# Optimization experiments

Measured on AMD Instinct MI355X. Metric: run time of the kernel, lower is better.

## Reference

```python
import jax, jax.numpy as jnp
import numpy as np
import math
from itertools import combinations

SEQ_LEN = 8
D_MODEL = 2048
OUT_DIM = 1152
WAY = 5
SHOT = 5
N_SUPPORT = WAY * SHOT
N_QUERIES = 200
TUPLES = np.array(list(combinations(range(SEQ_LEN), 2)), dtype=np.int32)  # [28, 2]
L = TUPLES.shape[0]  # 28 temporal tuples
PE_SCALE = 0.1
LN_EPS = 1e-5
COS_EPS = 1e-8


def _pos_encoding(seq, d):
    pos = jnp.arange(seq, dtype=jnp.float32)[:, None]
    div = jnp.exp(jnp.arange(0, d, 2, dtype=jnp.float32) * (-math.log(10000.0) / d))
    pe = jnp.zeros((seq, d), dtype=jnp.float32)
    pe = pe.at[:, 0::2].set(jnp.sin(pos * div) * PE_SCALE)
    pe = pe.at[:, 1::2].set(jnp.cos(pos * div) * PE_SCALE)
    return pe  # [seq, d]


def _layernorm(x, g, b):
    mu = x.mean(-1, keepdims=True)
    var = ((x - mu) ** 2).mean(-1, keepdims=True)
    return (x - mu) * jax.lax.rsqrt(var + LN_EPS) * g + b


def setup_inputs() -> dict:
    key = jax.random.key(0)
    ks = jax.random.split(key, 6)
    support_set = jax.random.normal(ks[0], (N_SUPPORT, SEQ_LEN, D_MODEL), jnp.float32)
    queries = jax.random.normal(ks[1], (N_QUERIES, SEQ_LEN, D_MODEL), jnp.float32)
    # sorted equal-shot episode: labels = [0]*5 + [1]*5 + ... + [4]*5
    support_labels = jnp.repeat(jnp.arange(WAY, dtype=jnp.int32), SHOT)
    k_w = jax.random.normal(ks[2], (OUT_DIM, 2 * D_MODEL), jnp.float32) * 0.02
    v_w = jax.random.normal(ks[3], (OUT_DIM, 2 * D_MODEL), jnp.float32) * 0.02
    k_b = jnp.zeros((OUT_DIM,), jnp.float32)
    v_b = jnp.zeros((OUT_DIM,), jnp.float32)
    ln_k_g = jnp.ones((OUT_DIM,), jnp.float32)
    ln_k_b = jnp.zeros((OUT_DIM,), jnp.float32)
    return {"support_set": support_set, "support_labels": support_labels,
            "queries": queries, "k_w": k_w, "k_b": k_b, "v_w": v_w, "v_b": v_b,
            "ln_k_g": ln_k_g, "ln_k_b": ln_k_b}


def reference(support_set, support_labels, queries, k_w, k_b, v_w, v_b, ln_k_g, ln_k_b):
    # dropout is inference-mode (identity)
    pe = _pos_encoding(SEQ_LEN, D_MODEL)
    sp = support_set + pe  # [Ns, S, D_MODEL]
    qp = queries + pe      # [Nq, S, D_MODEL]

    tup = jnp.asarray(TUPLES)
    # gather temporal tuples: [N, L, 2, D_MODEL] -> [N, L, 2*D_MODEL]
    s_t = sp[:, tup].reshape(N_SUPPORT, L, 2 * D_MODEL)
    q_t = qp[:, tup].reshape(N_QUERIES, L, 2 * D_MODEL)

    ks_s = _layernorm(s_t @ k_w.T + k_b, ln_k_g, ln_k_b)  # [Ns, L, OUT]
    ks_q = _layernorm(q_t @ k_w.T + k_b, ln_k_g, ln_k_b)  # [Nq, L, OUT]
    vs_s = s_t @ v_w.T + v_b                               # [Ns, L, OUT] (no norm, per original)
    vs_q = q_t @ v_w.T + v_b                               # [Nq, L, OUT]

    # labels are sorted equal-shot -> group by class via reshape
    ks_c = ks_s.reshape(WAY, SHOT, L, OUT_DIM)
    vs_c = vs_s.reshape(WAY, SHOT, L, OUT_DIM)

    # attention scores: [WAY, Nq, L(query tuple), SHOT, L(support tuple)]
    scores = jnp.einsum('qld,wsed->wqlse', ks_q, ks_c) / math.sqrt(OUT_DIM)
    attn = jax.nn.softmax(scores.reshape(WAY, N_QUERIES, L, SHOT * L), axis=-1)
    attn = attn.reshape(WAY, N_QUERIES, L, SHOT, L)
    # prototype: sum over shot of attn @ class_v -> [WAY, Nq, L, OUT]
    proto = jnp.einsum('wqlse,wsed->wqld', attn, vs_c)

    # query logits: -||q_v - proto||_F^2 / L per class
    diff = vs_q[None] - proto  # [WAY, Nq, L, OUT]
    ori = (-(diff ** 2).sum(axis=(-2, -1)) / L).T  # [Nq, WAY]

    # all_distances_tensor [Nq, L*OUT, WAY]
    A = jnp.transpose(proto, (1, 2, 3, 0)).reshape(N_QUERIES, L * OUT_DIM, WAY)
    num = jnp.einsum('qda,qdb->qab', A, A)            # [Nq, WAY, WAY]
    nrm = jnp.sqrt((A * A).sum(axis=1))               # [Nq, WAY]
    den = jnp.maximum(nrm[:, :, None] * nrm[:, None, :], COS_EPS)
    sim = num / den                                    # [Nq, WAY, WAY]
    return sim, ori
```

## Files before the change

kernel.cpp:

```cpp
#include <hip/hip_runtime.h>
#include <hip/hip_bf16.h>
#include <math.h>

typedef __hip_bfloat16 bf16;
typedef short s16x8 __attribute__((ext_vector_type(8)));
typedef float f32x4 __attribute__((ext_vector_type(4)));

#define NQ 200
#define SEQ 8
#define DM 2048
#define OUTD 1152
#define LT 28
#define M_ALL 6300
#define SM 5600
#define SN_PAD 768
#define ATT_STRIDE 720
#define N2 2304
#define KP 160
#define CH_Q 50
#define CH_ROWS 1400
#define CH_MPAD 1408
#define ABLK 144

__device__ __forceinline__ float bf2f(bf16 v) { return __bfloat162float(v); }
__device__ __forceinline__ bf16 f2bf(float v) { return __float2bfloat16(v); }
__device__ __forceinline__ float ubits2f(unsigned int u16) {
    unsigned int i = u16 << 16;
    float f; __builtin_memcpy(&f, &i, 4); return f;
}
__device__ __forceinline__ unsigned short f2bits(float f) {
    bf16 b = __float2bfloat16(f);
    unsigned short u; __builtin_memcpy(&u, &b, 2); return u;
}

__device__ const int TUP_A[LT] = {0,0,0,0,0,0,0,1,1,1,1,1,1,2,2,2,2,2,3,3,3,3,4,4,4,5,5,6};
__device__ const int TUP_B[LT] = {1,2,3,4,5,6,7,2,3,4,5,6,7,3,4,5,6,7,4,5,6,7,5,6,7,6,7,7};

__global__ __launch_bounds__(256) void wconv2_k(const float4* __restrict__ kw,
                                                const float4* __restrict__ vw,
                                                ushort4* __restrict__ o) {
    int i = blockIdx.x * 256 + threadIdx.x;
    float4 v = (i < 1179648) ? kw[i] : vw[i - 1179648];
    ushort4 r;
    r.x = f2bits(v.x); r.y = f2bits(v.y); r.z = f2bits(v.z); r.w = f2bits(v.w);
    o[i] = r;
}

__global__ __launch_bounds__(256) void pe_k(float* __restrict__ pe,
                                            bf16* __restrict__ attn_tail) {
    int i = blockIdx.x * 256 + threadIdx.x;
    int s = i >> 11, d = i & 2047;
    float dv = expf((float)(d & ~1) * (-9.210340371976184f / 2048.0f));
    float ang = (float)s * dv;
    pe[i] = (d & 1) ? cosf(ang) * 0.1f : sinf(ang) * 0.1f;
    for (int j = i; j < 32 * ATT_STRIDE; j += 64 * 256) attn_tail[j] = f2bf(0.f);
}

__global__ __launch_bounds__(256) void pex_k(const float* __restrict__ sup,
                                             const float* __restrict__ qry,
                                             const float* __restrict__ pe,
                                             bf16* __restrict__ pexb) {
    int r = blockIdx.x, t = threadIdx.x;
    int n, s;
    const float* src;
    if (r < 200) { n = r >> 3; s = r & 7; src = sup; }
    else { int rr = r - 200; n = rr >> 3; s = rr & 7; src = qry; }
    const float4* row = (const float4*)(src + ((size_t)n * SEQ + s) * DM);
    const float4* per = (const float4*)(pe + (size_t)s * DM);
    ushort4* orow = (ushort4*)(pexb + (size_t)r * DM);
    for (int d = t; d < DM / 4; d += 256) {
        float4 a = row[d], p = per[d];
        ushort4 o;
        o.x = f2bits(a.x + p.x); o.y = f2bits(a.y + p.y);
        o.z = f2bits(a.z + p.z); o.w = f2bits(a.w + p.w);
        orow[d] = o;
    }
}

__global__ __launch_bounds__(256) void gemm_bt(
    const bf16* __restrict__ A, int lda, size_t aZ,
    const bf16* __restrict__ B, int ldb, size_t bZ,
    float scale, bf16* __restrict__ C, int ldc, size_t cZ, int K, int mlim) {
    const int gx = gridDim.x, gy = gridDim.y;
    const int nwg = gx * gy * (int)gridDim.z;
    const int orig = ((int)blockIdx.z * gy + blockIdx.y) * gx + blockIdx.x;
    const int qc = nwg >> 3, rc = nwg & 7;
    const int xcd = orig & 7, sub = orig >> 3;
    const int lg = (xcd < rc ? xcd * (qc + 1) : rc * (qc + 1) + (xcd - rc) * qc) + sub;
    const int bx = lg % gx;
    const int rest = lg / gx;
    const int by = rest % gy, bz = rest / gy;

    const unsigned short* Ag0 = (const unsigned short*)A + aZ * bz;
    const unsigned short* Bg0 = (const unsigned short*)B + bZ * bz;
    const size_t cbase = cZ * bz;
    const int tile_m = bx * 128, tile_n = by * 128;
    __shared__ unsigned short A0s[4096];
    __shared__ unsigned short A1s[4096];
    __shared__ unsigned short B0s[4096];
    __shared__ unsigned short B1s[4096];
    const int t = threadIdx.x, lane = t & 63, wave = t >> 6;
    const int wm = (wave & 1) * 64, wn = (wave >> 1) * 64;
    const int srow = t >> 1, sq0 = (t & 1) * 2;
    const unsigned short* Ag = Ag0 + (size_t)(tile_m + srow) * lda + (t & 1) * 16;
    const unsigned short* Bg = Bg0 + (size_t)(tile_n + srow) * ldb + (t & 1) * 16;
    const int offW0 = ((sq0 + 0) * 128 + srow) * 8;
    const int offW1 = ((sq0 + 1) * 128 + srow) * 8;
    const int fr = lane & 15, quad = lane >> 4;

    f32x4 acc[4][4];
#pragma unroll
    for (int i = 0; i < 4; i++)
#pragma unroll
        for (int j = 0; j < 4; j++) acc[i][j] = {0.f, 0.f, 0.f, 0.f};

    uint4 ra0, ra1, rb0, rb1;
#define GLOAD(k0) do {                                                          \
    ra0 = *(const uint4*)(Ag + (k0));  ra1 = *(const uint4*)(Ag + (k0) + 8);    \
    rb0 = *(const uint4*)(Bg + (k0));  rb1 = *(const uint4*)(Bg + (k0) + 8);    \
  } while (0)

#define LDSW(AS, BS) do {                                                       \
    *(uint4*)&AS[offW0] = ra0; *(uint4*)&AS[offW1] = ra1;                       \
    *(uint4*)&BS[offW0] = rb0; *(uint4*)&BS[offW1] = rb1;                       \
  } while (0)

#define COMPUTE(AS, BS) do {                                                    \
    s16x8 af[4], bfv[4];                                                        \
    _Pragma("unroll")                                                           \
    for (int i = 0; i < 4; i++)                                                 \
        af[i] = *(const s16x8*)&AS[(quad * 128 + wm + i * 16 + fr) * 8];        \
    _Pragma("unroll")                                                           \
    for (int j = 0; j < 4; j++)                                                 \
        bfv[j] = *(const s16x8*)&BS[(quad * 128 + wn + j * 16 + fr) * 8];       \
    _Pragma("unroll")                                                           \
    for (int i = 0; i < 4; i++)                                                 \
    _Pragma("unroll")                                                           \
        for (int j = 0; j < 4; j++)                                             \
            acc[i][j] = __builtin_amdgcn_mfma_f32_16x16x32_bf16(af[i], bfv[j], acc[i][j], 0, 0, 0); \
  } while (0)

    const int nIter = K >> 5;
    GLOAD(0);
    LDSW(A0s, B0s);
    if (nIter > 1) GLOAD(32);
    __syncthreads();
    for (int s = 0; s < nIter; s += 2) {
        if (s + 1 < nIter) LDSW(A1s, B1s);
        if (s + 2 < nIter) GLOAD((s + 2) * 32);
        COMPUTE(A0s, B0s);
        __syncthreads();
        if (s + 1 < nIter) {
            if (s + 2 < nIter) LDSW(A0s, B0s);
            if (s + 3 < nIter) GLOAD((s + 3) * 32);
            COMPUTE(A1s, B1s);
            __syncthreads();
        }
    }
#undef GLOAD
#undef LDSW
#undef COMPUTE

    const int rb = quad * 4;
#pragma unroll
    for (int i = 0; i < 4; i++)
#pragma unroll
        for (int j = 0; j < 4; j++) {
            const int col = tile_n + wn + j * 16 + fr;
#pragma unroll
            for (int r = 0; r < 4; r++) {
                const int row = tile_m + wm + i * 16 + rb + r;
                if (row < mlim)
                    C[cbase + (size_t)row * ldc + col] = f2bf(acc[i][j][r] * scale);
            }
        }
}

__global__ __launch_bounds__(256) void combine_k(
    const unsigned int* __restrict__ Yk, const float* __restrict__ kb,
    const float* __restrict__ lng, const float* __restrict__ lnb,
    bf16* __restrict__ ks) {
    const int m = blockIdx.x, t = threadIdx.x, lane = t & 63, wave = t >> 6;
    int mm = m < 700 ? m : m - 700;
    int base = m < 700 ? 0 : 200;
    int nsamp = mm / LT, l = mm - nsamp * LT;
    const unsigned int* ya = Yk + (size_t)(base + nsamp * 8 + TUP_A[l]) * (N2 / 2);
    const unsigned int* yb = Yk + (size_t)(base + nsamp * 8 + TUP_B[l]) * (N2 / 2);
    float vals[5];
    int cnt = 0;
    float s = 0.f, s2 = 0.f;
    for (int n = t; n < OUTD; n += 256) {
        unsigned int ua = ya[n], ub = yb[n];
        float vk = ubits2f(ua & 0xFFFFu) + ubits2f(ub >> 16) + kb[n];
        vals[cnt++] = vk;
        s += vk; s2 += vk * vk;
    }
    for (int o = 32; o > 0; o >>= 1) { s += __shfl_xor(s, o); s2 += __shfl_xor(s2, o); }
    __shared__ float r1[4], r2[4];
    if (lane == 0) { r1[wave] = s; r2[wave] = s2; }
    __syncthreads();
    s = r1[0] + r1[1] + r1[2] + r1[3];
    s2 = r2[0] + r2[1] + r2[2] + r2[3];
    float mu = s * (1.f / OUTD);
    float var = s2 * (1.f / OUTD) - mu * mu;
    float inv = rsqrtf(fmaxf(var, 0.f) + 1e-5f);
    cnt = 0;
    for (int n = t; n < OUTD; n += 256)
        ks[(size_t)m * OUTD + n] = f2bf((vals[cnt++] - mu) * inv * lng[n] + lnb[n]);
}

__global__ __launch_bounds__(256) void combine_v(
    const unsigned int* __restrict__ Yv, const float* __restrict__ vb,
    bf16* __restrict__ vs) {
    const int m = blockIdx.x, t = threadIdx.x;
    int mm = m < 700 ? m : m - 700;
    int base = m < 700 ? 0 : 200;
    int nsamp = mm / LT, l = mm - nsamp * LT;
    const unsigned int* ya = Yv + (size_t)(base + nsamp * 8 + TUP_A[l]) * (N2 / 2);
    const unsigned int* yb = Yv + (size_t)(base + nsamp * 8 + TUP_B[l]) * (N2 / 2);
    for (int n = t; n < OUTD; n += 256) {
        unsigned int ua = ya[n], ub = yb[n];
        vs[(size_t)m * OUTD + n] =
            f2bf(ubits2f(ua & 0xFFFFu) + ubits2f(ub >> 16) + vb[n]);
    }
}

__global__ __launch_bounds__(320) void softmax_k(const bf16* __restrict__ sc,
                                                 bf16* __restrict__ attn) {
    const int row = blockIdx.x, w = threadIdx.x >> 6, lane = threadIdx.x & 63;
    const bf16* src = sc + (size_t)row * SN_PAD + w * 140;
    bf16* dst = attn + (size_t)row * ATT_STRIDE + w * ABLK;
    float a = bf2f(src[lane]);
    float b = bf2f(src[lane + 64]);
    float c = (lane < 12) ? bf2f(src[lane + 128]) : -3.0e38f;
    float m = fmaxf(fmaxf(a, b), c);
    for (int o = 32; o > 0; o >>= 1) m = fmaxf(m, __shfl_xor(m, o));
    float ea = __expf(a - m), eb = __expf(b - m);
    float ec = (lane < 12) ? __expf(c - m) : 0.f;
    float s = ea + eb + ec;
    for (int o = 32; o > 0; o >>= 1) s += __shfl_xor(s, o);
    float inv = 1.f / s;
    dst[lane] = f2bf(ea * inv);
    dst[lane + 64] = f2bf(eb * inv);
    if (lane < 16) dst[lane + 128] = f2bf(lane < 12 ? ec * inv : 0.f);
}

__global__ __launch_bounds__(256) void vspad_k(const bf16* __restrict__ vs,
                                               bf16* __restrict__ vp,
                                               float* __restrict__ gbuf) {
    int idx = blockIdx.x * 256 + threadIdx.x;
    if (blockIdx.x == 0)
        for (int i = threadIdx.x; i < NQ * 21; i += 256) gbuf[i] = 0.f;
    if (idx >= 5 * OUTD * KP) return;
    int j = idx % KP;
    int rest = idx / KP;
    int dcol = rest % OUTD;
    int w = rest / OUTD;
    vp[idx] = (j < 140) ? vs[(size_t)(w * 140 + j) * OUTD + dcol] : f2bf(0.f);
}

__global__ __launch_bounds__(256) void gramred_k(const bf16* __restrict__ protoc,
                                                 const bf16* __restrict__ vs,
                                                 float* __restrict__ gbuf,
                                                 int row0, int q0) {
    const int ql = blockIdx.x;
    const int lgb = blockIdx.y;
    const int t = threadIdx.x, lane = t & 63, wave = t >> 6;
    const size_t PZ = (size_t)CH_MPAD * OUTD;
    float g[15] = {0.f};
    float h[5] = {0.f, 0.f, 0.f, 0.f, 0.f};
    float e = 0.f;
    for (int idx = t; idx < 2 * OUTD / 8; idx += 256) {
        int li = idx / 144;
        int dv = idx - li * 144;
        int l = lgb * 2 + li;
        size_t ml = (size_t)(ql * LT + l) * OUTD + dv * 8;
        s16x8 pw0 = *(const s16x8*)&protoc[0 * PZ + ml];
        s16x8 pw1 = *(const s16x8*)&protoc[1 * PZ + ml];
        s16x8 pw2 = *(const s16x8*)&protoc[2 * PZ + ml];
        s16x8 pw3 = *(const s16x8*)&protoc[3 * PZ + ml];
        s16x8 pw4 = *(const s16x8*)&protoc[4 * PZ + ml];
        s16x8 vv = *(const s16x8*)&vs[(size_t)(700 + row0 + ql * LT + l) * OUTD + dv * 8];
#pragma unroll
        for (int ee = 0; ee < 8; ee++) {
            float pv[5];
            pv[0] = ubits2f((unsigned short)pw0[ee]);
            pv[1] = ubits2f((unsigned short)pw1[ee]);
            pv[2] = ubits2f((unsigned short)pw2[ee]);
            pv[3] = ubits2f((unsigned short)pw3[ee]);
            pv[4] = ubits2f((unsigned short)pw4[ee]);
            float v = ubits2f((unsigned short)vv[ee]);
            e += v * v;
            int c = 0;
#pragma unroll
            for (int a = 0; a < 5; a++) {
                h[a] += v * pv[a];
#pragma unroll
                for (int b = a; b < 5; b++) g[c++] += pv[a] * pv[b];
            }
        }
    }
    float vals[21];
#pragma unroll
    for (int k = 0; k < 15; k++) vals[k] = g[k];
#pragma unroll
    for (int k = 0; k < 5; k++) vals[15 + k] = h[k];
    vals[20] = e;
#pragma unroll
    for (int k = 0; k < 21; k++)
        for (int o = 32; o > 0; o >>= 1) vals[k] += __shfl_xor(vals[k], o);
    __shared__ float red[4][21];
    if (lane == 0)
#pragma unroll
        for (int k = 0; k < 21; k++) red[wave][k] = vals[k];
    __syncthreads();
    if (t < 21) {
        float s = red[0][t] + red[1][t] + red[2][t] + red[3][t];
        atomicAdd(&gbuf[(q0 + ql) * 21 + t], s);
    }
}

__global__ __launch_bounds__(64) void out_k(const float* __restrict__ gbuf,
                                            float* __restrict__ out) {
    int q = blockIdx.x;
    if (threadIdx.x != 0) return;
    const float* r = gbuf + q * 21;
    float G[5][5];
    int c = 0;
    for (int a = 0; a < 5; a++)
        for (int b = a; b < 5; b++) { G[a][b] = r[c]; G[b][a] = r[c]; c++; }
    float e = r[20];
    float nrm[5];
    for (int a = 0; a < 5; a++) nrm[a] = sqrtf(fmaxf(G[a][a], 0.f));
    for (int a = 0; a < 5; a++)
        for (int b = 0; b < 5; b++)
            out[(size_t)q * 25 + a * 5 + b] = G[a][b] / fmaxf(nrm[a] * nrm[b], 1e-8f);
    for (int w = 0; w < 5; w++)
        out[5000 + (size_t)q * 5 + w] = -(e - 2.f * r[15 + w] + G[w][w]) * (1.f / 28.f);
}

extern "C" void kernel_launch(void* const* d_in, const int* in_sizes, int n_in,
                              void* d_out, int out_size, void* d_ws, size_t ws_size,
                              hipStream_t stream) {
    const float* sup = (const float*)d_in[0];
    const float* qry = (const float*)d_in[2];
    const float* k_w = (const float*)d_in[3];
    const float* k_b = (const float*)d_in[4];
    const float* v_w = (const float*)d_in[5];
    const float* v_b = (const float*)d_in[6];
    const float* lng = (const float*)d_in[7];
    const float* lnb = (const float*)d_in[8];
    (void)in_sizes; (void)n_in; (void)out_size; (void)ws_size;

    char* ws = (char*)d_ws;
    bf16* pexb   = (bf16*)(ws + 0);
    bf16* wbf    = (bf16*)(ws + 7864320);
    bf16* Yk     = (bf16*)(ws + 26738688);
    bf16* Yv     = (bf16*)(ws + 35033088);
    bf16* ks     = (bf16*)(ws + 0);
    bf16* vs     = (bf16*)(ws + 16220160);
    bf16* sc     = (bf16*)(ws + 30735360);
    bf16* vsp    = (bf16*)(ws + 39386112);
    bf16* attn   = (bf16*)(ws + 41229312);
    float* gbuf  = (float*)(ws + 49339392);
    float* pe    = (float*)(ws + 49356192);
    bf16* protoc = (bf16*)(ws + 0);

    pe_k<<<dim3(64), dim3(256), 0, stream>>>(pe, attn + (size_t)SM * ATT_STRIDE);
    pex_k<<<dim3(1800), dim3(256), 0, stream>>>(sup, qry, pe, pexb);
    wconv2_k<<<dim3(9216), dim3(256), 0, stream>>>(
        (const float4*)k_w, (const float4*)v_w, (ushort4*)wbf);

    gemm_bt<<<dim3(15, 18, 2), dim3(256), 0, stream>>>(
        pexb, DM, 0, wbf, DM, (size_t)4718592,
        1.0f, Yk, N2, (size_t)4147200, DM, 1800);

    combine_k<<<dim3(M_ALL), dim3(256), 0, stream>>>(
        (const unsigned int*)Yk, k_b, lng, lnb, ks);
    combine_v<<<dim3(M_ALL), dim3(256), 0, stream>>>(
        (const unsigned int*)Yv, v_b, vs);

    gemm_bt<<<dim3(44, 6, 1), dim3(256), 0, stream>>>(
        ks + (size_t)700 * OUTD, OUTD, 0, ks, OUTD, 0,
        0.029462782549439484f, sc, SN_PAD, 0, OUTD, 5632);

    vspad_k<<<dim3((5 * OUTD * KP + 255) / 256), dim3(256), 0, stream>>>(
        vs, vsp, gbuf);
    softmax_k<<<dim3(SM), dim3(320), 0, stream>>>(sc, attn);

    for (int c = 0; c < 4; c++) {
        gemm_bt<<<dim3(11, 9, 5), dim3(256), 0, stream>>>(
            attn + (size_t)c * CH_ROWS * ATT_STRIDE, ATT_STRIDE, (size_t)ABLK,
            vsp, KP, (size_t)OUTD * KP,
            1.0f, protoc, OUTD, (size_t)CH_MPAD * OUTD, KP, CH_MPAD);
        gramred_k<<<dim3(CH_Q, 14), dim3(256), 0, stream>>>(
            protoc, vs, gbuf, c * CH_ROWS, c * CH_Q);
    }

    out_k<<<dim3(NQ), dim3(64), 0, stream>>>(gbuf, (float*)d_out);
}
```

Baseline: 343.8 us.

## Load GEMM MFMA fragments directly from global memory with triple-buffered registers

The bf16 GEMM no longer stages A/B tiles through LDS with barriers. Each wave now loads its MFMA operand fragments straight from global memory into registers and rotates through three register buffers so loads run ahead of compute. This removes LDS traffic and __syncthreads, but waves no longer share tile data, so global/L2 traffic roughly doubles (each A and B row is fetched by two waves). Register pressure also rises, which may reduce occupancy.

```diff
diff --git a/kernel.cpp b/kernel.cpp
--- a/kernel.cpp
+++ b/kernel.cpp
@@ -91,75 +91,60 @@
     const int rest = lg / gx;
     const int by = rest % gy, bz = rest / gy;
 
-    const unsigned short* Ag0 = (const unsigned short*)A + aZ * bz;
-    const unsigned short* Bg0 = (const unsigned short*)B + bZ * bz;
-    const size_t cbase = cZ * bz;
     const int tile_m = bx * 128, tile_n = by * 128;
-    __shared__ unsigned short A0s[4096];
-    __shared__ unsigned short A1s[4096];
-    __shared__ unsigned short B0s[4096];
-    __shared__ unsigned short B1s[4096];
     const int t = threadIdx.x, lane = t & 63, wave = t >> 6;
     const int wm = (wave & 1) * 64, wn = (wave >> 1) * 64;
-    const int srow = t >> 1, sq0 = (t & 1) * 2;
-    const unsigned short* Ag = Ag0 + (size_t)(tile_m + srow) * lda + (t & 1) * 16;
-    const unsigned short* Bg = Bg0 + (size_t)(tile_n + srow) * ldb + (t & 1) * 16;
-    const int offW0 = ((sq0 + 0) * 128 + srow) * 8;
-    const int offW1 = ((sq0 + 1) * 128 + srow) * 8;
     const int fr = lane & 15, quad = lane >> 4;
 
+    const unsigned short* Ab = (const unsigned short*)A + aZ * bz
+                               + (size_t)(tile_m + wm + fr) * lda + quad * 8;
+    const unsigned short* Bb = (const unsigned short*)B + bZ * bz
+                               + (size_t)(tile_n + wn + fr) * ldb + quad * 8;
+    const size_t a16 = (size_t)16 * lda, b16 = (size_t)16 * ldb;
+    const size_t cbase = cZ * bz;
+
     f32x4 acc[4][4];
 #pragma unroll
     for (int i = 0; i < 4; i++)
 #pragma unroll
         for (int j = 0; j < 4; j++) acc[i][j] = {0.f, 0.f, 0.f, 0.f};
 
-    uint4 ra0, ra1, rb0, rb1;
-#define GLOAD(k0) do {                                                          \
-    ra0 = *(const uint4*)(Ag + (k0));  ra1 = *(const uint4*)(Ag + (k0) + 8);    \
-    rb0 = *(const uint4*)(Bg + (k0));  rb1 = *(const uint4*)(Bg + (k0) + 8);    \
+    s16x8 pa[4], pb[4], qa[4], qb[4], ra_[4], rb_[4];
+
+#define LOADF(sa, sb, k0) do {                                                  \
+    _Pragma("unroll")                                                           \
+    for (int i = 0; i < 4; i++) {                                               \
+        sa[i] = *(const s16x8*)(Ab + (size_t)i * a16 + (size_t)(k0));           \
+        sb[i] = *(const s16x8*)(Bb + (size_t)i * b16 + (size_t)(k0));           \
+    }                                                                           \
   } while (0)
 
-#define LDSW(AS, BS) do {                                                       \
-    *(uint4*)&AS[offW0] = ra0; *(uint4*)&AS[offW1] = ra1;                       \
-    *(uint4*)&BS[offW0] = rb0; *(uint4*)&BS[offW1] = rb1;                       \
-  } while (0)
-
-#define COMPUTE(AS, BS) do {                                                    \
-    s16x8 af[4], bfv[4];                                                        \
-    _Pragma("unroll")                                                           \
-    for (int i = 0; i < 4; i++)                                                 \
-        af[i] = *(const s16x8*)&AS[(quad * 128 + wm + i * 16 + fr) * 8];        \
-    _Pragma("unroll")                                                           \
-    for (int j = 0; j < 4; j++)                                                 \
-        bfv[j] = *(const s16x8*)&BS[(quad * 128 + wn + j * 16 + fr) * 8];       \
+#define MM(sa, sb) do {                                                         \
     _Pragma("unroll")                                                           \
     for (int i = 0; i < 4; i++)                                                 \
     _Pragma("unroll")                                                           \
         for (int j = 0; j < 4; j++)                                             \
-            acc[i][j] = __builtin_amdgcn_mfma_f32_16x16x32_bf16(af[i], bfv[j], acc[i][j], 0, 0, 0); \
+            acc[i][j] = __builtin_amdgcn_mfma_f32_16x16x32_bf16(sa[i], sb[j], acc[i][j], 0, 0, 0); \
   } while (0)
 
     const int nIter = K >> 5;
-    GLOAD(0);
-    LDSW(A0s, B0s);
-    if (nIter > 1) GLOAD(32);
-    __syncthreads();
-    for (int s = 0; s < nIter; s += 2) {
-        if (s + 1 < nIter) LDSW(A1s, B1s);
-        if (s + 2 < nIter) GLOAD((s + 2) * 32);
-        COMPUTE(A0s, B0s);
-        __syncthreads();
+    LOADF(pa, pb, 0);
+    if (nIter > 1) LOADF(qa, qb, 32);
+    if (nIter > 2) LOADF(ra_, rb_, 64);
+    for (int s = 0; s < nIter; s += 3) {
+        MM(pa, pb);
+        if (s + 3 < nIter) LOADF(pa, pb, (s + 3) * 32);
         if (s + 1 < nIter) {
-            if (s + 2 < nIter) LDSW(A0s, B0s);
-            if (s + 3 < nIter) GLOAD((s + 3) * 32);
-            COMPUTE(A1s, B1s);
-            __syncthreads();
+            MM(qa, qb);
+            if (s + 4 < nIter) LOADF(qa, qb, (s + 4) * 32);
         }
-    }
-#undef GLOAD
-#undef LDSW
-#undef COMPUTE
+        if (s + 2 < nIter) {
+            MM(ra_, rb_);
+            if (s + 5 < nIter) LOADF(ra_, rb_, (s + 5) * 32);
+        }
+    }
+#undef LOADF
+#undef MM
 
     const int rb = quad * 4;
 #pragma unroll
```

Result: slower. 482.1 us (+40.2%).
